# Optimization experiments

Measured on AMD Instinct MI355X. Metric: run time of the kernel, lower is better.

The kernel has to match this reference:

```python
import jax, jax.numpy as jnp
import numpy as np

# --- physics constants (from source) ---
T_STALL = 5.4 * (1.0 / 100.0)
W_FREE = 1620.0 * (1.0 / 60.0) * 2.0 * np.pi
L_X = 0.129907
L_Y = 0.095724
A = L_X + L_Y
R = 4 * 0.0254
MASS = 6.0
INERTIA = MASS
MOMENT_OF_INERTIA = MASS * (12 * 0.0254) ** 2 / 6.0

LV2WV = np.array([[1, -1, -A], [1, 1, A], [1, 1, -A], [1, -1, A]], dtype=np.float32) / R  # [4,3]
CD2MD = np.array([[1, -1, -1], [1, 1, 1], [1, 1, -1], [1, -1, 1]], dtype=np.float32)      # [4,3]
WT2LA = (LV2WV.T / np.array([INERTIA, INERTIA, MOMENT_OF_INERTIA], dtype=np.float32)[:, None]).astype(np.float32)  # [3,4]

BATCH = 4_000_000


def _rot(c, s):
    # builds [..., 3, 3] = [[c,-s,0],[s,c,0],[0,0,1]]
    z = jnp.zeros_like(c)
    o = jnp.ones_like(c)
    return jnp.stack([
        jnp.stack([c, -s, z], axis=-1),
        jnp.stack([s, c, z], axis=-1),
        jnp.stack([z, z, o], axis=-1),
    ], axis=-2)


def setup_inputs() -> dict:
    key = jax.random.key(0)
    k1, k2 = jax.random.split(key)
    state = jax.random.normal(k1, (BATCH, 6), dtype=jnp.float32)
    control_duty = jax.random.normal(k2, (3,), dtype=jnp.float32)
    t = jnp.zeros((1,), dtype=jnp.float32)
    return {"t": t, "state": state, "control_duty": control_duty}


def reference(t, state, control_duty):
    lv2wv = jnp.asarray(LV2WV)
    cd2md = jnp.asarray(CD2MD)
    wt2la = jnp.asarray(WT2LA)

    absolute_vel = state[..., 3:]            # [..., 3]
    theta = state[..., 2]                    # [...]

    # absolute -> local frame
    a2l = _rot(jnp.cos(-theta), jnp.sin(-theta))                      # [...,3,3]
    local_vel = jnp.einsum('...ij,...j->...i', a2l, absolute_vel)     # [...,3]
    wheel_vel = jnp.einsum('ij,...j->...i', lv2wv, local_vel)         # [...,4]

    motor_duty = cd2md @ control_duty                                 # [4]
    is_same_direction = (jnp.sign(motor_duty * wheel_vel) + 1.0) / 2.0
    wheel_torque = T_STALL * (1.0 - jnp.abs(wheel_vel) * is_same_direction / W_FREE) * motor_duty  # [...,4]

    local_accel = jnp.einsum('ij,...j->...i', wt2la, wheel_torque)    # [...,3]

    # local -> absolute frame
    l2a = _rot(jnp.cos(theta), jnp.sin(theta))
    absolute_accel = jnp.einsum('...ij,...j->...i', l2a, local_accel)

    return jnp.concatenate([absolute_vel, absolute_accel], axis=-1)   # [...,6]
```

## Files before the change

### kernel.cpp

```cpp
#include <hip/hip_runtime.h>
#include <math.h>

namespace k {
constexpr double dA     = 0.129907 + 0.095724;
constexpr double dR     = 4.0 * 0.0254;
constexpr double dI     = 6.0;
constexpr double dMOI   = 6.0 * (12.0 * 0.0254) * (12.0 * 0.0254) / 6.0;
constexpr float T_STALL   = (float)(5.4 / 100.0);
constexpr float INV_WFREE = (float)(1.0 / (1620.0 / 60.0 * 2.0 * 3.14159265358979323846));
constexpr float A         = (float)dA;
constexpr float INV_R     = (float)(1.0 / dR);
constexpr float INV_RI    = (float)(1.0 / (dR * dI));
constexpr float A_RMOI    = (float)(dA / (dR * dMOI));
}

__device__ __forceinline__ float wheel_torque(float w, float m) {
    float p = m * w;
    float sgn = (float)(p > 0.0f) - (float)(p < 0.0f);
    float isd = 0.5f * (sgn + 1.0f);
    return k::T_STALL * (1.0f - fabsf(w) * isd * k::INV_WFREE) * m;
}

__device__ __forceinline__ void mecanum_elem(const float st[6],
                                             float m0, float m1, float m2, float m3,
                                             float o[6]) {
    float theta = st[2];
    float s, c;
    sincosf(theta, &s, &c);

    float v0 = st[3], v1 = st[4], v2 = st[5];

    float lv0 = c * v0 + s * v1;
    float lv1 = c * v1 - s * v0;

    float al2 = k::A * v2;
    float w0 = (lv0 - lv1 - al2) * k::INV_R;
    float w1 = (lv0 + lv1 + al2) * k::INV_R;
    float w2 = (lv0 + lv1 - al2) * k::INV_R;
    float w3 = (lv0 - lv1 + al2) * k::INV_R;

    float t0 = wheel_torque(w0, m0);
    float t1 = wheel_torque(w1, m1);
    float t2 = wheel_torque(w2, m2);
    float t3 = wheel_torque(w3, m3);

    float la0 = (t0 + t1 + t2 + t3) * k::INV_RI;
    float la1 = (-t0 + t1 + t2 - t3) * k::INV_RI;
    float la2 = (-t0 + t1 - t2 + t3) * k::A_RMOI;

    float aa0 = c * la0 - s * la1;
    float aa1 = s * la0 + c * la1;

    o[0] = st[3]; o[1] = st[4]; o[2] = st[5];
    o[3] = aa0; o[4] = aa1; o[5] = la2;
}

#define PAIRS_PER_BLOCK 256
#define F4_PER_BLOCK    (PAIRS_PER_BLOCK * 3)

__global__ __launch_bounds__(256) void mecanum_lds_kernel(
    const float4* __restrict__ state4,
    const float* __restrict__ cd,
    float4* __restrict__ out4,
    int n_pairs) {
    __shared__ float4 s_in[F4_PER_BLOCK];
    __shared__ float4 s_out[F4_PER_BLOCK];

    const int tid = threadIdx.x;
    const int pair_base = blockIdx.x * PAIRS_PER_BLOCK;
    const int f4_base = pair_base * 3;
    const int total4 = n_pairs * 3;

#pragma unroll
    for (int j = 0; j < 3; ++j) {
        int g = f4_base + j * 256 + tid;
        if (g < total4) s_in[j * 256 + tid] = state4[g];
    }

    float u0 = cd[0], u1 = cd[1], u2 = cd[2];
    float m0 = u0 - u1 - u2;
    float m1 = u0 + u1 + u2;
    float m2 = u0 + u1 - u2;
    float m3 = u0 - u1 + u2;

    __syncthreads();

    if (pair_base + tid < n_pairs) {
        float4 a = s_in[3 * tid + 0];
        float4 b = s_in[3 * tid + 1];
        float4 g = s_in[3 * tid + 2];

        float stA[6] = { a.x, a.y, a.z, a.w, b.x, b.y };
        float stB[6] = { b.z, b.w, g.x, g.y, g.z, g.w };
        float oA[6], oB[6];
        mecanum_elem(stA, m0, m1, m2, m3, oA);
        mecanum_elem(stB, m0, m1, m2, m3, oB);

        s_out[3 * tid + 0] = make_float4(oA[0], oA[1], oA[2], oA[3]);
        s_out[3 * tid + 1] = make_float4(oA[4], oA[5], oB[0], oB[1]);
        s_out[3 * tid + 2] = make_float4(oB[2], oB[3], oB[4], oB[5]);
    }

    __syncthreads();

#pragma unroll
    for (int j = 0; j < 3; ++j) {
        int g = f4_base + j * 256 + tid;
        if (g < total4) out4[g] = s_out[j * 256 + tid];
    }
}

__global__ void mecanum_tail_kernel(const float* __restrict__ state,
                                    const float* __restrict__ cd,
                                    float* __restrict__ out,
                                    int start, int n) {
    int i = start + blockIdx.x * blockDim.x + threadIdx.x;
    if (i >= n) return;
    float u0 = cd[0], u1 = cd[1], u2 = cd[2];
    float m0 = u0 - u1 - u2;
    float m1 = u0 + u1 + u2;
    float m2 = u0 + u1 - u2;
    float m3 = u0 - u1 + u2;
    float st[6], o[6];
#pragma unroll
    for (int j = 0; j < 6; ++j) st[j] = state[6 * i + j];
    mecanum_elem(st, m0, m1, m2, m3, o);
#pragma unroll
    for (int j = 0; j < 6; ++j) out[6 * i + j] = o[j];
}

extern "C" void kernel_launch(void* const* d_in, const int* in_sizes, int n_in,
                              void* d_out, int out_size, void* d_ws, size_t ws_size,
                              hipStream_t stream) {
    const float* state = (const float*)d_in[1];
    const float* cd    = (const float*)d_in[2];
    float* out         = (float*)d_out;

    int n = in_sizes[1] / 6;
    int n_pairs = n / 2;

    if (n_pairs > 0) {
        int grid = (n_pairs + PAIRS_PER_BLOCK - 1) / PAIRS_PER_BLOCK;
        mecanum_lds_kernel<<<grid, 256, 0, stream>>>(
            (const float4*)state, cd, (float4*)out, n_pairs);
    }
    if (n & 1) {
        mecanum_tail_kernel<<<1, 64, 0, stream>>>(state, cd, out, 2 * n_pairs, n);
    }
}
```

Before: 174.5 us.

## Use per-wave LDS staging with wave barriers and nontemporal stores

Each wavefront now stages and transposes only its own 192 float4 slice of shared memory, so block-wide __syncthreads become wave-level barriers. The input and output LDS buffers are merged into one, halving shared memory, and launch bounds request higher occupancy. Global output writes use nontemporal stores to avoid polluting cache. The risk is that the kernel is bandwidth bound, so removing barriers and shrinking LDS may change little.

```diff
diff --git a/kernel.cpp b/kernel.cpp
--- a/kernel.cpp
+++ b/kernel.cpp
@@ -13,6 +13,8 @@
 constexpr float INV_RI    = (float)(1.0 / (dR * dI));
 constexpr float A_RMOI    = (float)(dA / (dR * dMOI));
 }
+
+typedef float f32x4 __attribute__((ext_vector_type(4)));
 
 __device__ __forceinline__ float wheel_torque(float w, float m) {
     float p = m * w;
@@ -58,24 +60,20 @@
 #define PAIRS_PER_BLOCK 256
 #define F4_PER_BLOCK    (PAIRS_PER_BLOCK * 3)
 
-__global__ __launch_bounds__(256) void mecanum_lds_kernel(
+__global__ __launch_bounds__(256, 8) void mecanum_wave_kernel(
     const float4* __restrict__ state4,
     const float* __restrict__ cd,
     float4* __restrict__ out4,
     int n_pairs) {
-    __shared__ float4 s_in[F4_PER_BLOCK];
-    __shared__ float4 s_out[F4_PER_BLOCK];
+    __shared__ float4 s[F4_PER_BLOCK];
 
-    const int tid = threadIdx.x;
+    const int tid  = threadIdx.x;
+    const int wave = tid >> 6;
+    const int lane = tid & 63;
     const int pair_base = blockIdx.x * PAIRS_PER_BLOCK;
-    const int f4_base = pair_base * 3;
-    const int total4 = n_pairs * 3;
-
-#pragma unroll
-    for (int j = 0; j < 3; ++j) {
-        int g = f4_base + j * 256 + tid;
-        if (g < total4) s_in[j * 256 + tid] = state4[g];
-    }
+    const int f4_base   = pair_base * 3;
+    const int total4    = n_pairs * 3;
+    const int ws = wave * 192;
 
     float u0 = cd[0], u1 = cd[1], u2 = cd[2];
     float m0 = u0 - u1 - u2;
@@ -83,30 +81,42 @@
     float m2 = u0 + u1 - u2;
     float m3 = u0 - u1 + u2;
 
-    __syncthreads();
+#pragma unroll
+    for (int r = 0; r < 3; ++r) {
+        int g = f4_base + ws + r * 64 + lane;
+        if (g < total4) s[ws + r * 64 + lane] = state4[g];
+    }
+    __builtin_amdgcn_wave_barrier();
+    asm volatile("" ::: "memory");
 
-    if (pair_base + tid < n_pairs) {
-        float4 a = s_in[3 * tid + 0];
-        float4 b = s_in[3 * tid + 1];
-        float4 g = s_in[3 * tid + 2];
+    if (pair_base + wave * 64 + lane < n_pairs) {
+        float4 a  = s[ws + 3 * lane + 0];
+        float4 b  = s[ws + 3 * lane + 1];
+        float4 g4 = s[ws + 3 * lane + 2];
 
         float stA[6] = { a.x, a.y, a.z, a.w, b.x, b.y };
-        float stB[6] = { b.z, b.w, g.x, g.y, g.z, g.w };
+        float stB[6] = { b.z, b.w, g4.x, g4.y, g4.z, g4.w };
         float oA[6], oB[6];
         mecanum_elem(stA, m0, m1, m2, m3, oA);
         mecanum_elem(stB, m0, m1, m2, m3, oB);
 
-        s_out[3 * tid + 0] = make_float4(oA[0], oA[1], oA[2], oA[3]);
-        s_out[3 * tid + 1] = make_float4(oA[4], oA[5], oB[0], oB[1]);
-        s_out[3 * tid + 2] = make_float4(oB[2], oB[3], oB[4], oB[5]);
+        s[ws + 3 * lane + 0] = make_float4(oA[0], oA[1], oA[2], oA[3]);
+        s[ws + 3 * lane + 1] = make_float4(oA[4], oA[5], oB[0], oB[1]);
+        s[ws + 3 * lane + 2] = make_float4(oB[2], oB[3], oB[4], oB[5]);
     }
-
-    __syncthreads();
+    __builtin_amdgcn_wave_barrier();
+    asm volatile("" ::: "memory");
 
 #pragma unroll
-    for (int j = 0; j < 3; ++j) {
-        int g = f4_base + j * 256 + tid;
-        if (g < total4) out4[g] = s_out[j * 256 + tid];
+    for (int r = 0; r < 3; ++r) {
+        int idx = ws + r * 64 + lane;
+        int g = f4_base + idx;
+        if (g < total4) {
+            f32x4 v;
+            float4 t = s[idx];
+            v.x = t.x; v.y = t.y; v.z = t.z; v.w = t.w;
+            __builtin_nontemporal_store(v, (f32x4*)&out4[g]);
+        }
     }
 }
 
@@ -141,7 +151,7 @@
 
     if (n_pairs > 0) {
         int grid = (n_pairs + PAIRS_PER_BLOCK - 1) / PAIRS_PER_BLOCK;
-        mecanum_lds_kernel<<<grid, 256, 0, stream>>>(
+        mecanum_wave_kernel<<<grid, 256, 0, stream>>>(
             (const float4*)state, cd, (float4*)out, n_pairs);
     }
     if (n & 1) {
```

New measurement: 175.0 us. Within noise of the previous version (+0.3%).

## Replace LDS-staged pair kernel with direct per-element kernel and fast sincos

Applied to the files above, without the earlier changes.

Drops the shared-memory staging and the pairwise processing in favour of one thread per element. Each thread reads theta and velocity with one 16-byte vector load and writes the output with 16+8-byte stores. sincosf is replaced with the __sinf/__cosf intrinsics, and the separate odd-tail kernel is removed. This removes LDS traffic and barriers but relies on cache for strided, partly misaligned accesses, and it lowers trig accuracy.

```diff
diff --git a/kernel.cpp b/kernel.cpp
--- a/kernel.cpp
+++ b/kernel.cpp
@@ -14,6 +14,9 @@
 constexpr float A_RMOI    = (float)(dA / (dR * dMOI));
 }
 
+typedef float f32x4 __attribute__((ext_vector_type(4)));
+typedef float f32x2 __attribute__((ext_vector_type(2)));
+
 __device__ __forceinline__ float wheel_torque(float w, float m) {
     float p = m * w;
     float sgn = (float)(p > 0.0f) - (float)(p < 0.0f);
@@ -21,14 +24,26 @@
     return k::T_STALL * (1.0f - fabsf(w) * isd * k::INV_WFREE) * m;
 }
 
-__device__ __forceinline__ void mecanum_elem(const float st[6],
-                                             float m0, float m1, float m2, float m3,
-                                             float o[6]) {
-    float theta = st[2];
-    float s, c;
-    sincosf(theta, &s, &c);
+__global__ __launch_bounds__(256) void mecanum_direct_kernel(
+    const float* __restrict__ state,
+    const float* __restrict__ cd,
+    float* __restrict__ out,
+    int n) {
+    int i = blockIdx.x * 256 + threadIdx.x;
+    if (i >= n) return;
 
-    float v0 = st[3], v1 = st[4], v2 = st[5];
+    float u0 = cd[0], u1 = cd[1], u2 = cd[2];
+    float m0 = u0 - u1 - u2;
+    float m1 = u0 + u1 + u2;
+    float m2 = u0 + u1 - u2;
+    float m3 = u0 - u1 + u2;
+
+    f32x4 tv;
+    __builtin_memcpy(&tv, state + 6 * i + 2, 16);
+    float theta = tv.x, v0 = tv.y, v1 = tv.z, v2 = tv.w;
+
+    float s = __sinf(theta);
+    float c = __cosf(theta);
 
     float lv0 = c * v0 + s * v1;
     float lv1 = c * v1 - s * v0;
@@ -51,82 +66,10 @@
     float aa0 = c * la0 - s * la1;
     float aa1 = s * la0 + c * la1;
 
-    o[0] = st[3]; o[1] = st[4]; o[2] = st[5];
-    o[3] = aa0; o[4] = aa1; o[5] = la2;
-}
-
-#define PAIRS_PER_BLOCK 256
-#define F4_PER_BLOCK    (PAIRS_PER_BLOCK * 3)
-
-__global__ __launch_bounds__(256) void mecanum_lds_kernel(
-    const float4* __restrict__ state4,
-    const float* __restrict__ cd,
-    float4* __restrict__ out4,
-    int n_pairs) {
-    __shared__ float4 s_in[F4_PER_BLOCK];
-    __shared__ float4 s_out[F4_PER_BLOCK];
-
-    const int tid = threadIdx.x;
-    const int pair_base = blockIdx.x * PAIRS_PER_BLOCK;
-    const int f4_base = pair_base * 3;
-    const int total4 = n_pairs * 3;
-
-#pragma unroll
-    for (int j = 0; j < 3; ++j) {
-        int g = f4_base + j * 256 + tid;
-        if (g < total4) s_in[j * 256 + tid] = state4[g];
-    }
-
-    float u0 = cd[0], u1 = cd[1], u2 = cd[2];
-    float m0 = u0 - u1 - u2;
-    float m1 = u0 + u1 + u2;
-    float m2 = u0 + u1 - u2;
-    float m3 = u0 - u1 + u2;
-
-    __syncthreads();
-
-    if (pair_base + tid < n_pairs) {
-        float4 a = s_in[3 * tid + 0];
-        float4 b = s_in[3 * tid + 1];
-        float4 g = s_in[3 * tid + 2];
-
-        float stA[6] = { a.x, a.y, a.z, a.w, b.x, b.y };
-        float stB[6] = { b.z, b.w, g.x, g.y, g.z, g.w };
-        float oA[6], oB[6];
-        mecanum_elem(stA, m0, m1, m2, m3, oA);
-        mecanum_elem(stB, m0, m1, m2, m3, oB);
-
-        s_out[3 * tid + 0] = make_float4(oA[0], oA[1], oA[2], oA[3]);
-        s_out[3 * tid + 1] = make_float4(oA[4], oA[5], oB[0], oB[1]);
-        s_out[3 * tid + 2] = make_float4(oB[2], oB[3], oB[4], oB[5]);
-    }
-
-    __syncthreads();
-
-#pragma unroll
-    for (int j = 0; j < 3; ++j) {
-        int g = f4_base + j * 256 + tid;
-        if (g < total4) out4[g] = s_out[j * 256 + tid];
-    }
-}
-
-__global__ void mecanum_tail_kernel(const float* __restrict__ state,
-                                    const float* __restrict__ cd,
-                                    float* __restrict__ out,
-                                    int start, int n) {
-    int i = start + blockIdx.x * blockDim.x + threadIdx.x;
-    if (i >= n) return;
-    float u0 = cd[0], u1 = cd[1], u2 = cd[2];
-    float m0 = u0 - u1 - u2;
-    float m1 = u0 + u1 + u2;
-    float m2 = u0 + u1 - u2;
-    float m3 = u0 - u1 + u2;
-    float st[6], o[6];
-#pragma unroll
-    for (int j = 0; j < 6; ++j) st[j] = state[6 * i + j];
-    mecanum_elem(st, m0, m1, m2, m3, o);
-#pragma unroll
-    for (int j = 0; j < 6; ++j) out[6 * i + j] = o[j];
+    f32x4 o1; o1.x = v0; o1.y = v1; o1.z = v2; o1.w = aa0;
+    __builtin_memcpy(out + 6 * i, &o1, 16);
+    f32x2 o2; o2.x = aa1; o2.y = la2;
+    __builtin_memcpy(out + 6 * i + 4, &o2, 8);
 }
 
 extern "C" void kernel_launch(void* const* d_in, const int* in_sizes, int n_in,
@@ -137,14 +80,9 @@
     float* out         = (float*)d_out;
 
     int n = in_sizes[1] / 6;
-    int n_pairs = n / 2;
 
-    if (n_pairs > 0) {
-        int grid = (n_pairs + PAIRS_PER_BLOCK - 1) / PAIRS_PER_BLOCK;
-        mecanum_lds_kernel<<<grid, 256, 0, stream>>>(
-            (const float4*)state, cd, (float4*)out, n_pairs);
-    }
-    if (n & 1) {
-        mecanum_tail_kernel<<<1, 64, 0, stream>>>(state, cd, out, 2 * n_pairs, n);
+    if (n > 0) {
+        int grid = (n + 255) / 256;
+        mecanum_direct_kernel<<<grid, 256, 0, stream>>>(state, cd, out, n);
     }
 }
```

Result: no change. 175.0 us, median of 2 (+0.3%).
